# Kernel tuning notes

Hardware: AMD Instinct MI355X
Metric: run time of the kernel (lower is better)

## Reference

```python
import jax, jax.numpy as jnp
import numpy as np

D_MODEL = 4096
N_HEAD = 32
N_KV_HEAD = 8
D_HEAD = D_MODEL // N_HEAD  # 128
B, T = 2, 2048


def setup_inputs() -> dict:
    key = jax.random.key(0)
    ks = jax.random.split(key, 6)
    x = jax.random.normal(ks[0], (B, T, D_MODEL), dtype=jnp.float32)
    # RoPE angles: theta_i = 10000^(-2i/d_head), angle = pos * theta_i
    inv_freq = 1.0 / (10000.0 ** (jnp.arange(0, D_HEAD, 2, dtype=jnp.float32) / D_HEAD))
    angles = jnp.arange(T, dtype=jnp.float32)[:, None] * inv_freq[None, :]  # [T, D_HEAD//2]
    freqs_cos = jnp.cos(angles)
    freqs_sin = jnp.sin(angles)
    s = 0.02
    wq = jax.random.normal(ks[1], (D_MODEL, N_HEAD * D_HEAD), dtype=jnp.float32) * s
    wk = jax.random.normal(ks[2], (D_MODEL, N_KV_HEAD * D_HEAD), dtype=jnp.float32) * s
    wv = jax.random.normal(ks[3], (D_MODEL, N_KV_HEAD * D_HEAD), dtype=jnp.float32) * s
    wo = jax.random.normal(ks[4], (D_MODEL, D_MODEL), dtype=jnp.float32) * s
    return {"x": x, "freqs_cos": freqs_cos, "freqs_sin": freqs_sin,
            "wq": wq, "wk": wk, "wv": wv, "wo": wo}


def _apply_rope(xq, xk, cos, sin):
    # xq: [B,T,Hq,D], xk: [B,T,Hk,D]; cos/sin: [T, D//2]
    def rot(t):
        tr = t.astype(jnp.float32).reshape(*t.shape[:-1], -1, 2)  # [B,T,H,D//2,2]
        xr, xi = tr[..., 0], tr[..., 1]
        c = cos[None, :, None, :]
        s = sin[None, :, None, :]
        out_r = xr * c - xi * s
        out_i = xr * s + xi * c
        return jnp.stack([out_r, out_i], axis=-1).reshape(t.shape).astype(t.dtype)
    return rot(xq), rot(xk)


def reference(x, freqs_cos, freqs_sin, wq, wk, wv, wo):
    Bq, Tq, _ = x.shape
    xq = (x @ wq).reshape(Bq, Tq, N_HEAD, D_HEAD)
    xk = (x @ wk).reshape(Bq, Tq, N_KV_HEAD, D_HEAD)
    xv = (x @ wv).reshape(Bq, Tq, N_KV_HEAD, D_HEAD)
    xq, xk = _apply_rope(xq, xk, freqs_cos, freqs_sin)
    # [B,H,T,D]
    xq = xq.transpose(0, 2, 1, 3)
    xk = xk.transpose(0, 2, 1, 3)
    xv = xv.transpose(0, 2, 1, 3)
    # GQA: repeat kv heads
    rep = N_HEAD // N_KV_HEAD
    xk = jnp.repeat(xk, rep, axis=1)
    xv = jnp.repeat(xv, rep, axis=1)
    scale = 1.0 / np.sqrt(D_HEAD)
    scores = jnp.einsum("bhqd,bhkd->bhqk", xq, xk) * scale
    causal = jnp.tril(jnp.ones((Tq, Tq), dtype=bool))
    scores = jnp.where(causal[None, None], scores, jnp.finfo(scores.dtype).min)
    probs = jax.nn.softmax(scores, axis=-1)
    z = jnp.einsum("bhqk,bhkd->bhqd", probs, xv)
    z = z.transpose(0, 2, 1, 3).reshape(Bq, Tq, D_MODEL)
    return z @ wo
```

## Files before the change

### kernel.cpp

```cpp
#include <hip/hip_runtime.h>

typedef unsigned short u16;
typedef unsigned int u32;
typedef u16 u16x8 __attribute__((ext_vector_type(8)));
typedef __bf16 bf16x8 __attribute__((ext_vector_type(8)));
typedef float f32x4 __attribute__((ext_vector_type(4)));

#define TOKENS 4096
#define DMODEL 4096
#define QKVN 6144
#define NHEAD 32
#define NKV 8
#define DHEAD 128
#define SEQ 2048

__device__ inline u16 f2bf(float f) {
    unsigned int u = __float_as_uint(f);
    u += 0x7fffu + ((u >> 16) & 1u);
    return (u16)(u >> 16);
}
__device__ inline float bf2f(u16 h) {
    return __uint_as_float(((unsigned int)h) << 16);
}
__device__ inline u32 pack2bf(float a, float b) {
    return (u32)f2bf(a) | ((u32)f2bf(b) << 16);
}
__device__ inline f32x4 mfma16(bf16x8 a, bf16x8 b, f32x4 c) {
    return __builtin_amdgcn_mfma_f32_16x16x32_bf16(a, b, c, 0, 0, 0);
}
__device__ __forceinline__ void gload16(const u16* g, u16* l) {
    __builtin_amdgcn_global_load_lds((const __attribute__((address_space(1))) u32*)g,
                                     (__attribute__((address_space(3))) u32*)l, 16, 0, 0);
}

__global__ __launch_bounds__(256) void f2bf_kernel(const float* __restrict__ in,
                                                   u16* __restrict__ out, int n) {
    int i = (blockIdx.x * 256 + threadIdx.x) * 4;
    if (i >= n) return;
    float4 v = *(const float4*)(in + i);
    u16 o0 = f2bf(v.x), o1 = f2bf(v.y), o2 = f2bf(v.z), o3 = f2bf(v.w);
    u16* p = out + i;
    p[0] = o0; p[1] = o1; p[2] = o2; p[3] = o3;
}

__global__ __launch_bounds__(256) void transpose_kernel(const float* __restrict__ in,
                                                        u16* __restrict__ out,
                                                        int K, int N) {
    __shared__ float t[32][33];
    int n0 = blockIdx.x * 32, k0 = blockIdx.y * 32;
    int x = threadIdx.x, y = threadIdx.y;
#pragma unroll
    for (int i = 0; i < 4; i++)
        t[y + 8 * i][x] = in[(size_t)(k0 + y + 8 * i) * N + n0 + x];
    __syncthreads();
#pragma unroll
    for (int i = 0; i < 4; i++)
        out[(size_t)(n0 + y + 8 * i) * K + k0 + x] = f2bf(t[x][y + 8 * i]);
}

__global__ __launch_bounds__(256) void vtrans_kernel(const u16* __restrict__ qkv,
                                                     u16* __restrict__ vt) {
    __shared__ u16 t[32][33];
    int b = blockIdx.z;
    int c0 = blockIdx.x * 32;
    int r0 = blockIdx.y * 32;
    int x = threadIdx.x, y = threadIdx.y;
    const u16* in = qkv + (size_t)(b * SEQ) * QKVN + 5120;
#pragma unroll
    for (int i = 0; i < 4; i++)
        t[y + 8 * i][x] = in[(size_t)(r0 + y + 8 * i) * QKVN + c0 + x];
    __syncthreads();
    u16* out = vt + (size_t)b * 1024 * SEQ;
#pragma unroll
    for (int i = 0; i < 4; i++)
        out[(size_t)(c0 + y + 8 * i) * SEQ + r0 + x] = t[x][y + 8 * i];
}

template <bool OUT_F32>
__global__ __launch_bounds__(256, 2) void gemm_lds(const u16* __restrict__ A,
                                                   const u16* __restrict__ Bt,
                                                   void* __restrict__ C,
                                                   int M, int N, int K) {
    __shared__ u16 lA[128 * 32];
    __shared__ u16 lB[128 * 32];
    int tid = threadIdx.x, wave = tid >> 6, lane = tid & 63;
    int quad = lane >> 4, l16 = lane & 15;
    int m0 = blockIdx.y * 128, n0 = blockIdx.x * 128;
    int wm = (wave >> 1) * 64, wn = (wave & 1) * 64;
    int lrow = lane >> 2, lcol = (lane & 3) * 8;

    const u16* ga = A + (size_t)(m0 + wave * 32 + lrow) * K + lcol;
    const u16* gb = Bt + (size_t)(n0 + wave * 32 + lrow) * K + lcol;
    u16* la = lA + (wave * 32) * 32;
    u16* lb = lB + (wave * 32) * 32;

    f32x4 acc[4][4] = {};

    gload16(ga, la);
    gload16(ga + (size_t)16 * K, la + 512);
    gload16(gb, lb);
    gload16(gb + (size_t)16 * K, lb + 512);

    for (int k0 = 0; k0 < K; k0 += 32) {
        __syncthreads();
        bf16x8 af[4], bfr[4];
#pragma unroll
        for (int i = 0; i < 4; i++)
            af[i] = *(const bf16x8*)(lA + (wm + i * 16 + l16) * 32 + quad * 8);
#pragma unroll
        for (int j = 0; j < 4; j++)
            bfr[j] = *(const bf16x8*)(lB + (wn + j * 16 + l16) * 32 + quad * 8);
        if (k0 + 32 < K) {
            __syncthreads();
            gload16(ga + k0 + 32, la);
            gload16(ga + (size_t)16 * K + k0 + 32, la + 512);
            gload16(gb + k0 + 32, lb);
            gload16(gb + (size_t)16 * K + k0 + 32, lb + 512);
        }
#pragma unroll
        for (int i = 0; i < 4; i++)
#pragma unroll
            for (int j = 0; j < 4; j++)
                acc[i][j] = mfma16(af[i], bfr[j], acc[i][j]);
    }

#pragma unroll
    for (int i = 0; i < 4; i++)
#pragma unroll
        for (int j = 0; j < 4; j++) {
            int row = m0 + wm + i * 16 + quad * 4;
            int col = n0 + wn + j * 16 + l16;
            if (OUT_F32) {
                float* Cf = (float*)C;
#pragma unroll
                for (int r = 0; r < 4; r++)
                    Cf[(size_t)(row + r) * N + col] = acc[i][j][r];
            } else {
                u16* Cb = (u16*)C;
#pragma unroll
                for (int r = 0; r < 4; r++)
                    Cb[(size_t)(row + r) * N + col] = f2bf(acc[i][j][r]);
            }
        }
}

__global__ __launch_bounds__(256) void rope2_kernel(u16* __restrict__ buf,
                                                    const float* __restrict__ cosb,
                                                    const float* __restrict__ sinb,
                                                    int nheads, int colbase, float scale) {
    int idx = blockIdx.x * 256 + threadIdx.x;
    int p = idx & 63;
    int rest = idx >> 6;
    int h = rest & (nheads - 1);
    int tok = rest / nheads;
    int tseq = tok & (SEQ - 1);
    float c = cosb[tseq * 64 + p], s = sinb[tseq * 64 + p];
    u32* ptr = (u32*)(buf + (size_t)tok * QKVN + colbase + h * DHEAD + 2 * p);
    u32 v = *ptr;
    float xr = bf2f((u16)(v & 0xffff)), xi = bf2f((u16)(v >> 16));
    float orr = (xr * c - xi * s) * scale;
    float oii = (xr * s + xi * c) * scale;
    *ptr = pack2bf(orr, oii);
}

#define LDP 72
#define NINF (-__builtin_inff())

__global__ __launch_bounds__(256, 2) void flash2_kernel(const u16* __restrict__ QKV,
                                                        const u16* __restrict__ Vt,
                                                        u16* __restrict__ Z) {
    __shared__ u16 lK[4][64 * 32];
    __shared__ u16 lV[2][128 * 32];
    __shared__ u16 lP[4][32 * LDP];
    int tid = threadIdx.x, wave = tid >> 6, lane = tid & 63;
    int quad = lane >> 4, l16 = lane & 15;
    int qt = 15 - (int)blockIdx.x;
    int h = blockIdx.y, b = blockIdx.z;
    int kvh = h >> 2;
    int Q0 = qt * 128;
    int qw = Q0 + wave * 32;
    int lrow = lane >> 2, lcol = (lane & 3) * 8;

    bf16x8 qf[2][4];
#pragma unroll
    for (int nt = 0; nt < 2; nt++) {
        const u16* qp = QKV + (size_t)(b * SEQ + qw + nt * 16 + l16) * QKVN + h * DHEAD;
#pragma unroll
        for (int kk = 0; kk < 4; kk++)
            qf[nt][kk] = *(const bf16x8*)(qp + kk * 32 + quad * 8);
    }

    f32x4 o[2][8] = {};
    float mrun[2] = {NINF, NINF};
    float lrun[2] = {0.f, 0.f};

    const u16* gk = QKV + (size_t)(b * SEQ + lrow) * QKVN + DMODEL + kvh * DHEAD + wave * 32 + lcol;
    u16* lk = lK[wave];
    int kf_w = wave >> 1, dh_w = (wave & 1) * 64;
    const u16* gv = Vt + ((size_t)(b * NKV + kvh) * DHEAD + dh_w + lrow) * SEQ + kf_w * 32 + lcol;
    u16* lv = lV[kf_w] + dh_w * 32;

    int nkt = 2 * qt + 2;
    for (int kt = 0; kt < nkt; kt++) {
        int key0 = kt * 64;
        if (kt) __syncthreads();
#pragma unroll
        for (int g = 0; g < 4; g++)
            gload16(gk + (size_t)(key0 + g * 16) * QKVN, lk + g * 512);
#pragma unroll
        for (int g = 0; g < 4; g++)
            gload16(gv + (size_t)(g * 16) * SEQ + key0, lv + g * 512);
        __syncthreads();

        if (key0 <= qw + 31) {
            f32x4 st[4][2] = {};
#pragma unroll
            for (int kk = 0; kk < 4; kk++) {
                bf16x8 kfr[4];
#pragma unroll
                for (int mt = 0; mt < 4; mt++)
                    kfr[mt] = *(const bf16x8*)(lK[kk] + (mt * 16 + l16) * 32 + quad * 8);
#pragma unroll
                for (int mt = 0; mt < 4; mt++)
#pragma unroll
                    for (int nt = 0; nt < 2; nt++)
                        st[mt][nt] = mfma16(kfr[mt], qf[nt][kk], st[mt][nt]);
            }
            if (key0 + 63 > qw) {
#pragma unroll
                for (int mt = 0; mt < 4; mt++)
#pragma unroll
                    for (int nt = 0; nt < 2; nt++)
#pragma unroll
                        for (int r = 0; r < 4; r++)
                            if (key0 + mt * 16 + quad * 4 + r > qw + nt * 16 + l16)
                                st[mt][nt][r] = NINF;
            }
            float alpha[2];
#pragma unroll
            for (int nt = 0; nt < 2; nt++) {
                float vmax = NINF;
#pragma unroll
                for (int mt = 0; mt < 4; mt++)
#pragma unroll
                    for (int r = 0; r < 4; r++) vmax = fmaxf(vmax, st[mt][nt][r]);
                vmax = fmaxf(vmax, __shfl_xor(vmax, 16));
                vmax = fmaxf(vmax, __shfl_xor(vmax, 32));
                float mnew = fmaxf(mrun[nt], vmax);
                alpha[nt] = __expf(mrun[nt] - mnew);
                mrun[nt] = mnew;
                float rsum = 0.f;
#pragma unroll
                for (int mt = 0; mt < 4; mt++)
#pragma unroll
                    for (int r = 0; r < 4; r++) {
                        float p = __expf(st[mt][nt][r] - mnew);
                        st[mt][nt][r] = p;
                        rsum += p;
                    }
                rsum += __shfl_xor(rsum, 16);
                rsum += __shfl_xor(rsum, 32);
                lrun[nt] = lrun[nt] * alpha[nt] + rsum;
#pragma unroll
                for (int mt = 0; mt < 4; mt++) {
                    u32 p01 = pack2bf(st[mt][nt][0], st[mt][nt][1]);
                    u32 p23 = pack2bf(st[mt][nt][2], st[mt][nt][3]);
                    uint2 pk; pk.x = p01; pk.y = p23;
                    *(uint2*)(lP[wave] + (nt * 16 + l16) * LDP + mt * 16 + quad * 4) = pk;
                }
            }
#pragma unroll
            for (int mtq = 0; mtq < 2; mtq++)
#pragma unroll
                for (int r = 0; r < 4; r++) {
                    float av = __shfl(alpha[mtq], quad * 4 + r);
#pragma unroll
                    for (int ntd = 0; ntd < 8; ntd++) o[mtq][ntd][r] *= av;
                }
#pragma unroll
            for (int kfi = 0; kfi < 2; kfi++) {
                bf16x8 pf0 = *(const bf16x8*)(lP[wave] + l16 * LDP + kfi * 32 + quad * 8);
                bf16x8 pf1 = *(const bf16x8*)(lP[wave] + (16 + l16) * LDP + kfi * 32 + quad * 8);
#pragma unroll
                for (int ntd = 0; ntd < 8; ntd++) {
                    bf16x8 vfr = *(const bf16x8*)(lV[kfi] + (ntd * 16 + l16) * 32 + quad * 8);
                    o[0][ntd] = mfma16(pf0, vfr, o[0][ntd]);
                    o[1][ntd] = mfma16(pf1, vfr, o[1][ntd]);
                }
            }
        }
    }
#pragma unroll
    for (int mtq = 0; mtq < 2; mtq++) {
        float linv[4];
#pragma unroll
        for (int r = 0; r < 4; r++) linv[r] = 1.0f / __shfl(lrun[mtq], quad * 4 + r);
#pragma unroll
        for (int ntd = 0; ntd < 8; ntd++)
#pragma unroll
            for (int r = 0; r < 4; r++) {
                int q = qw + mtq * 16 + quad * 4 + r;
                Z[(size_t)(b * SEQ + q) * DMODEL + h * DHEAD + ntd * 16 + l16] =
                    f2bf(o[mtq][ntd][r] * linv[r]);
            }
    }
}

extern "C" void kernel_launch(void* const* d_in, const int* in_sizes, int n_in,
                              void* d_out, int out_size, void* d_ws, size_t ws_size,
                              hipStream_t stream) {
    const float* x    = (const float*)d_in[0];
    const float* fcos = (const float*)d_in[1];
    const float* fsin = (const float*)d_in[2];
    const float* wq   = (const float*)d_in[3];
    const float* wk   = (const float*)d_in[4];
    const float* wv   = (const float*)d_in[5];
    const float* wo   = (const float*)d_in[6];
    float* out = (float*)d_out;
    char* ws = (char*)d_ws;

    const size_t MiB = 1024ull * 1024ull;
    u16* xb    = (u16*)(ws);
    u16* zb    = xb;
    u16* wqkvt = (u16*)(ws + 32 * MiB);
    u16* wot   = (u16*)(ws + 80 * MiB);
    u16* qkv   = (u16*)(ws + 112 * MiB);
    u16* vtb   = (u16*)(ws + 160 * MiB);

    f2bf_kernel<<<16384, 256, 0, stream>>>(x, xb, TOKENS * DMODEL);
    dim3 tb(32, 8);
    transpose_kernel<<<dim3(128, 128), tb, 0, stream>>>(wq, wqkvt, 4096, 4096);
    transpose_kernel<<<dim3(32, 128), tb, 0, stream>>>(wk, wqkvt + (size_t)4096 * 4096, 4096, 1024);
    transpose_kernel<<<dim3(32, 128), tb, 0, stream>>>(wv, wqkvt + (size_t)5120 * 4096, 4096, 1024);
    transpose_kernel<<<dim3(128, 128), tb, 0, stream>>>(wo, wot, 4096, 4096);

    gemm_lds<false><<<dim3(48, 32), 256, 0, stream>>>(xb, wqkvt, qkv, 4096, QKVN, 4096);

    rope2_kernel<<<32768, 256, 0, stream>>>(qkv, fcos, fsin, NHEAD, 0, 0.08838834764831845f);
    rope2_kernel<<<8192, 256, 0, stream>>>(qkv, fcos, fsin, NKV, DMODEL, 1.0f);

    vtrans_kernel<<<dim3(32, 64, 2), tb, 0, stream>>>(qkv, vtb);

    flash2_kernel<<<dim3(16, 32, 2), 256, 0, stream>>>(qkv, vtb, zb);

    gemm_lds<true><<<dim3(32, 32), 256, 0, stream>>>(zb, wot, out, 4096, 4096, 4096);
}
```

Measured before the change: 849.9 us.

## Replace 128x128 GEMM with 256x256 double-buffered pipelined 8-wave GEMM

Both projection GEMMs now use a 256x256 block tile with 8 waves and a K-step of 64. LDS is double-buffered and XOR-swizzled, and loads are interleaved with MFMA phases under manual barriers, vmcnt waits and s_setprio. The aim is more data reuse per block, less LDS bank conflict, and hiding global-load latency behind compute. In exchange the kernel needs many more registers and 128KB of LDS, and the small grids (384 and 256 blocks) may underfill the CUs.

New measurement: 768.0 us. 9.6% less time.

```diff
diff --git a/kernel.cpp b/kernel.cpp
--- a/kernel.cpp
+++ b/kernel.cpp
@@ -13,6 +13,10 @@
 #define NKV 8
 #define DHEAD 128
 #define SEQ 2048
+
+#define BARRIER() asm volatile("s_barrier" ::: "memory")
+#define LGKM0() asm volatile("s_waitcnt lgkmcnt(0)" ::: "memory")
+#define VMCNT(n) asm volatile("s_waitcnt vmcnt(" #n ")" ::: "memory")
 
 __device__ inline u16 f2bf(float f) {
     unsigned int u = __float_as_uint(f);
@@ -77,59 +81,132 @@
 }
 
 template <bool OUT_F32>
-__global__ __launch_bounds__(256, 2) void gemm_lds(const u16* __restrict__ A,
-                                                   const u16* __restrict__ Bt,
-                                                   void* __restrict__ C,
-                                                   int M, int N, int K) {
-    __shared__ u16 lA[128 * 32];
-    __shared__ u16 lB[128 * 32];
-    int tid = threadIdx.x, wave = tid >> 6, lane = tid & 63;
-    int quad = lane >> 4, l16 = lane & 15;
-    int m0 = blockIdx.y * 128, n0 = blockIdx.x * 128;
-    int wm = (wave >> 1) * 64, wn = (wave & 1) * 64;
-    int lrow = lane >> 2, lcol = (lane & 3) * 8;
-
-    const u16* ga = A + (size_t)(m0 + wave * 32 + lrow) * K + lcol;
-    const u16* gb = Bt + (size_t)(n0 + wave * 32 + lrow) * K + lcol;
-    u16* la = lA + (wave * 32) * 32;
-    u16* lb = lB + (wave * 32) * 32;
-
-    f32x4 acc[4][4] = {};
-
-    gload16(ga, la);
-    gload16(ga + (size_t)16 * K, la + 512);
-    gload16(gb, lb);
-    gload16(gb + (size_t)16 * K, lb + 512);
-
-    for (int k0 = 0; k0 < K; k0 += 32) {
-        __syncthreads();
-        bf16x8 af[4], bfr[4];
-#pragma unroll
-        for (int i = 0; i < 4; i++)
-            af[i] = *(const bf16x8*)(lA + (wm + i * 16 + l16) * 32 + quad * 8);
-#pragma unroll
-        for (int j = 0; j < 4; j++)
-            bfr[j] = *(const bf16x8*)(lB + (wn + j * 16 + l16) * 32 + quad * 8);
-        if (k0 + 32 < K) {
-            __syncthreads();
-            gload16(ga + k0 + 32, la);
-            gload16(ga + (size_t)16 * K + k0 + 32, la + 512);
-            gload16(gb + k0 + 32, lb);
-            gload16(gb + (size_t)16 * K + k0 + 32, lb + 512);
+__global__ __launch_bounds__(512, 2) void gemm256(const u16* __restrict__ A,
+                                                  const u16* __restrict__ Bt,
+                                                  void* __restrict__ C,
+                                                  int M, int N, int K) {
+    __shared__ u16 lds[2][2][2][128 * 64];
+    const int tid = threadIdx.x, wave = tid >> 6, lane = tid & 63;
+    const int quad = lane >> 4, l16 = lane & 15;
+    const int wave_m = wave >> 2, wave_n = wave & 3;
+    const int m0 = blockIdx.y * 256, n0 = blockIdx.x * 256;
+    const int wn = wave_n * 64;
+    const int nk = K >> 6;
+
+    const int srow = wave * 16 + (lane >> 3);
+    const int scol = ((lane & 7) ^ (lane >> 3)) << 3;
+    const u16* ga0 = A + (size_t)(m0 + srow) * K + scol;
+    const u16* gb0 = Bt + (size_t)(n0 + srow) * K + scol;
+
+    auto STAGE = [&](int op, int buf, int half, int kt) {
+        const u16* src = (op ? gb0 : ga0) + (size_t)(half * 128) * K + (kt << 6);
+        u16* dst = &lds[op][buf][half][wave * 1024];
+        gload16(src, dst);
+        gload16(src + (size_t)8 * K, dst + 512);
+    };
+    auto FRAG = [&](const u16* base, int lr, int c) -> bf16x8 {
+        int idx = (lr * 64 + c) ^ ((lr & 7) << 3);
+        return *(const bf16x8*)(base + idx);
+    };
+
+    f32x4 acc[8][4] = {};
+
+    STAGE(1, 0, 0, 0); STAGE(1, 0, 1, 0); STAGE(0, 0, 0, 0); STAGE(0, 0, 1, 0);
+    STAGE(1, 1, 0, 1); STAGE(1, 1, 1, 1); STAGE(0, 1, 0, 1);
+    VMCNT(6);
+    BARRIER();
+
+    bf16x8 af[4][2], bfr[4][2];
+
+    auto KTILE = [&](int kt, int cur) {
+        const int nxt = cur ^ 1;
+        const int k1 = kt + 1 < nk ? kt + 1 : nk - 1;
+        const int k2 = kt + 2 < nk ? kt + 2 : nk - 1;
+        const u16* aB = &lds[0][cur][wave_m][0];
+#pragma unroll
+        for (int i = 0; i < 4; i++)
+#pragma unroll
+            for (int kk = 0; kk < 2; kk++)
+                af[i][kk] = FRAG(aB, i * 16 + l16, kk * 32 + quad * 8);
+#pragma unroll
+        for (int j = 0; j < 4; j++) {
+            const int brow = wn + j * 16;
+            const u16* bB = &lds[1][cur][brow >> 7][0];
+#pragma unroll
+            for (int kk = 0; kk < 2; kk++)
+                bfr[j][kk] = FRAG(bB, (brow & 127) + l16, kk * 32 + quad * 8);
         }
-#pragma unroll
-        for (int i = 0; i < 4; i++)
-#pragma unroll
-            for (int j = 0; j < 4; j++)
-                acc[i][j] = mfma16(af[i], bfr[j], acc[i][j]);
+        STAGE(0, nxt, 1, k1);
+        BARRIER();
+        __builtin_amdgcn_s_setprio(1);
+#pragma unroll
+        for (int i = 0; i < 4; i++)
+#pragma unroll
+            for (int j = 0; j < 2; j++)
+#pragma unroll
+                for (int kk = 0; kk < 2; kk++)
+                    acc[i][j] = mfma16(af[i][kk], bfr[j][kk], acc[i][j]);
+        __builtin_amdgcn_s_setprio(0);
+        LGKM0();
+        BARRIER();
+        STAGE(1, cur, 0, k2);
+        BARRIER();
+        __builtin_amdgcn_s_setprio(1);
+#pragma unroll
+        for (int i = 0; i < 4; i++)
+#pragma unroll
+            for (int j = 0; j < 2; j++)
+#pragma unroll
+                for (int kk = 0; kk < 2; kk++)
+                    acc[i][2 + j] = mfma16(af[i][kk], bfr[2 + j][kk], acc[i][2 + j]);
+        __builtin_amdgcn_s_setprio(0);
+        BARRIER();
+#pragma unroll
+        for (int i = 0; i < 4; i++)
+#pragma unroll
+            for (int kk = 0; kk < 2; kk++)
+                af[i][kk] = FRAG(aB, 64 + i * 16 + l16, kk * 32 + quad * 8);
+        STAGE(1, cur, 1, k2);
+        BARRIER();
+        __builtin_amdgcn_s_setprio(1);
+#pragma unroll
+        for (int i = 0; i < 4; i++)
+#pragma unroll
+            for (int j = 0; j < 2; j++)
+#pragma unroll
+                for (int kk = 0; kk < 2; kk++)
+                    acc[4 + i][j] = mfma16(af[i][kk], bfr[j][kk], acc[4 + i][j]);
+        __builtin_amdgcn_s_setprio(0);
+        LGKM0();
+        BARRIER();
+        STAGE(0, cur, 0, k2);
+        BARRIER();
+        __builtin_amdgcn_s_setprio(1);
+#pragma unroll
+        for (int i = 0; i < 4; i++)
+#pragma unroll
+            for (int j = 0; j < 2; j++)
+#pragma unroll
+                for (int kk = 0; kk < 2; kk++)
+                    acc[4 + i][2 + j] = mfma16(af[i][kk], bfr[2 + j][kk], acc[4 + i][2 + j]);
+        __builtin_amdgcn_s_setprio(0);
+        VMCNT(6);
+        BARRIER();
+    };
+
+    for (int kt = 0; kt < nk; kt += 2) {
+        KTILE(kt, 0);
+        KTILE(kt + 1, 1);
     }
 
-#pragma unroll
-    for (int i = 0; i < 4; i++)
+    VMCNT(0);
+
+#pragma unroll
+    for (int i = 0; i < 8; i++)
 #pragma unroll
         for (int j = 0; j < 4; j++) {
-            int row = m0 + wm + i * 16 + quad * 4;
-            int col = n0 + wn + j * 16 + l16;
+            const int row = m0 + wave_m * 128 + i * 16 + quad * 4;
+            const int col = n0 + wn + j * 16 + l16;
             if (OUT_F32) {
                 float* Cf = (float*)C;
 #pragma unroll
@@ -334,7 +411,7 @@
     transpose_kernel<<<dim3(32, 128), tb, 0, stream>>>(wv, wqkvt + (size_t)5120 * 4096, 4096, 1024);
     transpose_kernel<<<dim3(128, 128), tb, 0, stream>>>(wo, wot, 4096, 4096);
 
-    gemm_lds<false><<<dim3(48, 32), 256, 0, stream>>>(xb, wqkvt, qkv, 4096, QKVN, 4096);
+    gemm256<false><<<dim3(24, 16), 512, 0, stream>>>(xb, wqkvt, qkv, 4096, QKVN, 4096);
 
     rope2_kernel<<<32768, 256, 0, stream>>>(qkv, fcos, fsin, NHEAD, 0, 0.08838834764831845f);
     rope2_kernel<<<8192, 256, 0, stream>>>(qkv, fcos, fsin, NKV, DMODEL, 1.0f);
@@ -343,5 +420,5 @@
 
     flash2_kernel<<<dim3(16, 32, 2), 256, 0, stream>>>(qkv, vtb, zb);
 
-    gemm_lds<true><<<dim3(32, 32), 256, 0, stream>>>(zb, wot, out, 4096, 4096, 4096);
-}
+    gemm256<true><<<dim3(16, 16), 512, 0, stream>>>(zb, wot, out, 4096, 4096, 4096);
+}
```
